# Performance work log

Measured on AMD Instinct MI355X. Metric: run time of the kernel, lower is better.

## Reference

```python
import jax, jax.numpy as jnp
import numpy as np

B, H, S, D = 4, 16, 2048, 64
SCALE = 8.0  # sqrt(D)
NEG = -1000000000.0


def setup_inputs() -> dict:
    key = jax.random.key(0)
    kq, kk, kv = jax.random.split(key, 3)
    q = jax.random.normal(kq, (B, H, S, D), dtype=jnp.float32)
    k = jax.random.normal(kk, (B, H, S, D), dtype=jnp.float32)
    v = jax.random.normal(kv, (B, H, S, D), dtype=jnp.float32)
    # causal mask: True means masked out (matches torch masked_fill)
    mask = jnp.triu(jnp.ones((S, S), dtype=bool), k=1)[None, None, :, :]
    mask = jnp.broadcast_to(mask, (B, 1, S, S))
    return {"q": q, "k": k, "v": v, "mask": mask}


def reference(q, k, v, mask):
    # score = q @ k^T / scale  -> [B,H,S,S]
    score = jnp.einsum("bhqd,bhkd->bhqk", q, k) / SCALE
    score = jnp.where(mask, NEG, score)
    probs = jax.nn.softmax(score, axis=-1)
    context = jnp.einsum("bhqk,bhkd->bhqd", probs, v)
    return context
```

## Files before the change

kernel.cpp:

```cpp
#include <hip/hip_runtime.h>

#define SQ 2048
#define DH 64
#define BK 64
#define NQT 32
#define NBH 64
#define M0 8.0f

#define WS_BYTES ((size_t)2 * NBH * SQ * DH * 2)

typedef float f32x4 __attribute__((ext_vector_type(4)));
typedef __bf16 bf16x8 __attribute__((ext_vector_type(8)));
typedef _Float16 f16x4 __attribute__((ext_vector_type(4)));
typedef _Float16 f16x8 __attribute__((ext_vector_type(8)));
typedef __fp16 fp16x2 __attribute__((ext_vector_type(2)));
typedef unsigned short u16x8 __attribute__((ext_vector_type(8)));
typedef unsigned int u32x4 __attribute__((ext_vector_type(4)));

#define WAIT_VM(N) asm volatile("s_waitcnt vmcnt(" #N ")" ::: "memory")

static __device__ __forceinline__ unsigned int pkbf(float a, float b) {
#if __has_builtin(__builtin_amdgcn_cvt_pk_bf16_f32)
  typedef __bf16 bf16x2 __attribute__((ext_vector_type(2)));
  bf16x2 r = __builtin_amdgcn_cvt_pk_bf16_f32(a, b);
  return __builtin_bit_cast(unsigned int, r);
#else
  unsigned int ua = __builtin_bit_cast(unsigned int, a);
  unsigned int ub = __builtin_bit_cast(unsigned int, b);
  ua += 0x7fffu + ((ua >> 16) & 1u);
  ub += 0x7fffu + ((ub >> 16) & 1u);
  return (ua >> 16) | (ub & 0xffff0000u);
#endif
}

static __device__ __forceinline__ unsigned int pkf16(float a, float b) {
  fp16x2 r = __builtin_amdgcn_cvt_pkrtz(a, b);
  return __builtin_bit_cast(unsigned int, r);
}

static __device__ __forceinline__ f32x4 mfma_qk(u16x8 a, u16x8 b, f32x4 c) {
  return __builtin_amdgcn_mfma_f32_16x16x32_bf16(
      __builtin_bit_cast(bf16x8, a), __builtin_bit_cast(bf16x8, b), c, 0, 0, 0);
}

static __device__ __forceinline__ f32x4 mfma_pv(f16x4 a, f16x4 b, f32x4 c) {
  return __builtin_amdgcn_mfma_f32_16x16x16f16(a, b, c, 0, 0, 0);
}

static __device__ __forceinline__ f32x4 mfma_pv32(f16x8 a, f16x8 b, f32x4 c) {
  return __builtin_amdgcn_mfma_f32_16x16x32_f16(a, b, c, 0, 0, 0);
}

static __device__ __forceinline__ void ld16(unsigned short* l, const unsigned short* g) {
  __builtin_amdgcn_global_load_lds(
      (const __attribute__((address_space(1))) unsigned int*)(const void*)g,
      (__attribute__((address_space(3))) unsigned int*)(void*)l, 16, 0, 0);
}

static __device__ __forceinline__ void store_tile(float* wb, float* dst,
                                                  const f32x4* o, int lane,
                                                  int l15, int quad) {
#pragma unroll
  for (int dt = 0; dt < 4; ++dt) {
    const int colw = dt * 16 + quad * 4;
    *(f32x4*)&wb[l15 * 64 + (colw ^ ((l15 & 3) * 16))] = o[dt];
  }
  __builtin_amdgcn_wave_barrier();
#pragma unroll
  for (int j = 0; j < 4; ++j) {
    const int row = j * 4 + (lane >> 4);
    const int colw = (lane & 15) * 4;
    f32x4 v = *(const f32x4*)&wb[row * 64 + (colw ^ ((row & 3) * 16))];
    *(f32x4*)&dst[row * 64 + colw] = v;
  }
}

__global__ __launch_bounds__(256) void prep(const float* __restrict__ K,
                                            const float* __restrict__ V,
                                            unsigned short* __restrict__ Kf,
                                            unsigned short* __restrict__ Vf) {
  const int bh = (int)blockIdx.x >> 5;
  const int st = (int)blockIdx.x & 31;
  const int tid = threadIdx.x;
  __shared__ __align__(16) unsigned short T[DH * 64];
  {
    const int kvb = (tid >> 4) * 4, vdb = (tid & 15) * 4;
    const float* vp = V + ((size_t)bh * SQ + st * 64 + kvb) * DH + vdb;
    f32x4 r0 = *(const f32x4*)vp, r1 = *(const f32x4*)(vp + DH),
          r2 = *(const f32x4*)(vp + 2 * DH), r3 = *(const f32x4*)(vp + 3 * DH);
    const int uu = kvb >> 3, h = (kvb >> 2) & 1;
#pragma unroll
    for (int i = 0; i < 4; ++i) {
      const int d = vdb + i;
      uint2 w = {pkf16(r0[i], r1[i]), pkf16(r2[i], r3[i])};
      *(uint2*)&T[d * 64 + ((uu ^ (d & 7)) * 8) + h * 4] = w;
    }
  }
  {
    const size_t kin = ((size_t)bh * SQ + st * 64) * DH;
    unsigned short* kfo = Kf + (size_t)bh * SQ * DH + (size_t)st * 64 * DH;
#pragma unroll
    for (int e = 0; e < 2; ++e) {
      const int L = tid * 2 + e;
      const int l15 = L & 15, quad = (L >> 4) & 3, c = (L >> 6) & 1, nt = (L >> 7) & 3;
      const int krow = (nt >> 1) * 32 + ((l15 >> 2) & 3) * 8 + (nt & 1) * 4 + (l15 & 3);
      const float* kp = K + kin + (size_t)krow * DH + (c * 4 + quad) * 8;
      f32x4 x = *(const f32x4*)kp, y = *(const f32x4*)(kp + 4);
      u32x4 w = {pkbf(x[0], x[1]), pkbf(x[2], x[3]), pkbf(y[0], y[1]), pkbf(y[2], y[3])};
      *(u32x4*)&kfo[L * 8] = w;
    }
  }
  __syncthreads();
  {
    unsigned short* vfo = Vf + (size_t)bh * SQ * DH + (size_t)st * 64 * DH;
#pragma unroll
    for (int e = 0; e < 2; ++e) {
      const int L = tid * 2 + e;
      const int l15 = L & 15, quad = (L >> 4) & 3, dt = (L >> 6) & 3, n2 = (L >> 8) & 1;
      const int d = dt * 16 + l15, uu = n2 * 4 + quad;
      u16x8 val = *(const u16x8*)&T[d * 64 + ((uu ^ (d & 7)) * 8)];
      *(u16x8*)&vfo[L * 8] = val;
    }
  }
}

__global__ __launch_bounds__(256, 2) void fa_main(
    const float* __restrict__ Q, const unsigned short* __restrict__ Kf,
    const unsigned short* __restrict__ Vf, float* __restrict__ O) {
  const int lin = (int)blockIdx.x;
  const int xcd = lin & 7, u = lin >> 3;
  const int hh = u & 7, j = u >> 3;
  const int bh = hh * 8 + xcd;

  const int tid = threadIdx.x;
  const int wv = tid >> 6;
  const int lane = tid & 63;
  const int l15 = lane & 15;
  const int quad = lane >> 4;

  const int p0 = j * 4 + wv;

  __shared__ __align__(16) unsigned short KS[4][2][4096];

  const size_t hq = (size_t)bh * (SQ * DH);
  const unsigned short* KfH = Kf + (size_t)bh * SQ * DH;
  const unsigned short* VfH = Vf + (size_t)bh * SQ * DH;

  const f16x8 ones8 = {(_Float16)1.f, (_Float16)1.f, (_Float16)1.f, (_Float16)1.f,
                       (_Float16)1.f, (_Float16)1.f, (_Float16)1.f, (_Float16)1.f};

  auto stageK = [&](int slot, int t) {
#pragma unroll
    for (int i = 0; i < 8; ++i)
      ld16(&KS[wv][slot][i * 512 + lane * 8],
           &KfH[(size_t)t * 4096 + i * 512 + lane * 8]);
  };

  auto run = [&](int s) {
    const int sg = s >> 1;
    const int qb = s * 32;
    const int qo = (s & 1) * 32;

    u16x8 qf[2][2];
    {
      const float scq = 0.125f * 1.4426950408889634f;
#pragma unroll
      for (int f = 0; f < 2; ++f) {
        const float* qp = Q + hq + (size_t)(qb + 16 * f + l15) * DH + quad * 8;
#pragma unroll
        for (int c = 0; c < 2; ++c) {
          f32x4 x = *(const f32x4*)(qp + c * 32);
          f32x4 y = *(const f32x4*)(qp + c * 32 + 4);
          u32x4 w = {pkbf(x[0] * scq, x[1] * scq), pkbf(x[2] * scq, x[3] * scq),
                     pkbf(y[0] * scq, y[1] * scq), pkbf(y[2] * scq, y[3] * scq)};
          qf[f][c] = __builtin_bit_cast(u16x8, w);
        }
      }
    }

    f32x4 o0[4], o1[4], la0, la1;
#pragma unroll
    for (int dt = 0; dt < 4; ++dt) {
      o0[dt] = (f32x4){0.f, 0.f, 0.f, 0.f};
      o1[dt] = (f32x4){0.f, 0.f, 0.f, 0.f};
    }
    la0 = (f32x4){0.f, 0.f, 0.f, 0.f};
    la1 = (f32x4){0.f, 0.f, 0.f, 0.f};

    f16x8 vb[8];
    auto loadV = [&](int t) {
#pragma unroll
      for (int i = 0; i < 8; ++i)
        vb[i] = *(const f16x8*)&VfH[(size_t)t * 4096 + i * 512 + lane * 8];
    };

    auto attend = [&](const unsigned short* Ks, bool diag) {
      f32x4 s0[4], s1[4];
#pragma unroll
      for (int nt = 0; nt < 4; ++nt) {
        f32x4 a0 = {-M0, -M0, -M0, -M0}, a1 = {-M0, -M0, -M0, -M0};
#pragma unroll
        for (int c = 0; c < 2; ++c) {
          u16x8 kf = *(const u16x8*)&Ks[(nt * 2 + c) * 512 + lane * 8];
          a0 = mfma_qk(kf, qf[0][c], a0);
          a1 = mfma_qk(kf, qf[1][c], a1);
        }
        s0[nt] = a0;
        s1[nt] = a1;
      }
      if (diag) {
#pragma unroll
        for (int nt = 0; nt < 4; ++nt)
#pragma unroll
          for (int r = 0; r < 4; ++r) {
            const int kvl = (nt >> 1) * 32 + quad * 8 + (nt & 1) * 4 + r;
            if (kvl > qo + l15) s0[nt][r] = -1e30f;
            if (kvl > qo + 16 + l15) s1[nt][r] = -1e30f;
          }
      }
      f16x8 pf0[2], pf1[2];
#pragma unroll
      for (int n2 = 0; n2 < 2; ++n2) {
        f32x4 pe0, po0, pe1, po1;
#pragma unroll
        for (int r = 0; r < 4; ++r) {
          pe0[r] = __builtin_amdgcn_exp2f(s0[2 * n2][r]);
          po0[r] = __builtin_amdgcn_exp2f(s0[2 * n2 + 1][r]);
          pe1[r] = __builtin_amdgcn_exp2f(s1[2 * n2][r]);
          po1[r] = __builtin_amdgcn_exp2f(s1[2 * n2 + 1][r]);
        }
        u32x4 w0 = {pkf16(pe0[0], pe0[1]), pkf16(pe0[2], pe0[3]),
                    pkf16(po0[0], po0[1]), pkf16(po0[2], po0[3])};
        u32x4 w1 = {pkf16(pe1[0], pe1[1]), pkf16(pe1[2], pe1[3]),
                    pkf16(po1[0], po1[1]), pkf16(po1[2], po1[3])};
        pf0[n2] = __builtin_bit_cast(f16x8, w0);
        pf1[n2] = __builtin_bit_cast(f16x8, w1);
      }
#pragma unroll
      for (int n2 = 0; n2 < 2; ++n2) {
        la0 = mfma_pv32(ones8, pf0[n2], la0);
        la1 = mfma_pv32(ones8, pf1[n2], la1);
      }
#pragma unroll
      for (int dt = 0; dt < 4; ++dt) {
#pragma unroll
        for (int n2 = 0; n2 < 2; ++n2) {
          const f16x8 vf = vb[n2 * 4 + dt];
          o0[dt] = mfma_pv32(vf, pf0[n2], o0[dt]);
          o1[dt] = mfma_pv32(vf, pf1[n2], o1[dt]);
        }
      }
    };

    stageK(0, 0);
    loadV(0);
    if (sg >= 1) stageK(1, 1);

    for (int t = 0; t <= sg; ++t) {
      if (t < sg) {
        WAIT_VM(8);
      } else {
        WAIT_VM(0);
      }
      __builtin_amdgcn_sched_barrier(0);
      attend(&KS[wv][t & 1][0], t == sg);
      __builtin_amdgcn_sched_barrier(0);
      if (t + 1 <= sg) loadV(t + 1);
      if (t + 2 <= sg) stageK(t & 1, t + 2);
    }

    {
      const float inv0 = 1.0f / la0[0];
      const float inv1 = 1.0f / la1[0];
#pragma unroll
      for (int f = 0; f < 2; ++f) {
        const f32x4* oo = f ? o1 : o0;
        const float inv = f ? inv1 : inv0;
        float* dst = O + hq + (size_t)(qb + f * 16 + l15) * DH + quad * 4;
#pragma unroll
        for (int dt = 0; dt < 4; ++dt) {
          f32x4 v = oo[dt] * inv;
          *(f32x4*)(dst + dt * 16) = v;
        }
      }
    }
  };

  run(p0);
  run(63 - p0);
}

__global__ __launch_bounds__(256, 4) void fa_full(
    const float* __restrict__ Q, const float* __restrict__ K,
    const float* __restrict__ V, float* __restrict__ O) {
  const int lin = (int)blockIdx.x;
  const int xcd = lin & 7;
  const int u = lin >> 3;
  const int hh = u & 7;
  const int p = u >> 3;
  const int bh = hh * 8 + xcd;
  const int tid = threadIdx.x;
  const int wv = tid >> 6;
  const int lane = tid & 63;
  const int l15 = lane & 15;
  const int quad = lane >> 4;
  __shared__ __align__(16) unsigned short SMEM[2][2 * BK * DH];
  const size_t hbase = (size_t)bh * (SQ * DH);
  const int krr = tid >> 3, kcc = (tid & 7) * 8;
  const int kvb = (tid >> 4) * 4, vdb = (tid & 15) * 4;
#pragma unroll
  for (int ph = 0; ph < 2; ++ph) {
    const int qt = ph ? (NQT - 1 - p) : p;
    const int wq0 = qt * 64 + wv * 16;
    u16x8 qf[2];
    {
      const float scq = 0.125f * 1.4426950408889634f;
      const float* qp = Q + hbase + (size_t)(wq0 + l15) * DH + quad * 8;
#pragma unroll
      for (int c = 0; c < 2; ++c) {
        f32x4 x = *(const f32x4*)(qp + c * 32);
        f32x4 y = *(const f32x4*)(qp + c * 32 + 4);
        u32x4 w = {pkbf(x[0] * scq, x[1] * scq), pkbf(x[2] * scq, x[3] * scq),
                   pkbf(y[0] * scq, y[1] * scq), pkbf(y[2] * scq, y[3] * scq)};
        qf[c] = __builtin_bit_cast(u16x8, w);
      }
    }
    f32x4 o[4];
#pragma unroll
    for (int dt = 0; dt < 4; ++dt) o[dt] = (f32x4){0.f, 0.f, 0.f, 0.f};
    float l = 0.f;
    f32x4 ka[2][2], va[4];
    {
      const float* kp = K + hbase + (size_t)krr * DH + kcc;
      ka[0][0] = *(const f32x4*)kp;             ka[0][1] = *(const f32x4*)(kp + 4);
      ka[1][0] = *(const f32x4*)(kp + 32 * DH); ka[1][1] = *(const f32x4*)(kp + 32 * DH + 4);
      const float* vp = V + hbase + (size_t)kvb * DH + vdb;
      va[0] = *(const f32x4*)vp;            va[1] = *(const f32x4*)(vp + DH);
      va[2] = *(const f32x4*)(vp + 2 * DH); va[3] = *(const f32x4*)(vp + 3 * DH);
    }
    __syncthreads();
    {
      unsigned short* Ksn = SMEM[0];
      unsigned short* Vsn = SMEM[0] + BK * DH;
#pragma unroll
      for (int h = 0; h < 2; ++h) {
        const int rr = h * 32 + krr;
        u32x4 w = {pkbf(ka[h][0][0], ka[h][0][1]), pkbf(ka[h][0][2], ka[h][0][3]),
                   pkbf(ka[h][1][0], ka[h][1][1]), pkbf(ka[h][1][2], ka[h][1][3])};
        *(u32x4*)&Ksn[rr * DH + (kcc ^ ((rr & 7) * 8))] = w;
      }
#pragma unroll
      for (int i = 0; i < 4; ++i) {
        const int d = vdb + i;
        uint2 w = {pkf16(va[0][i], va[1][i]), pkf16(va[2][i], va[3][i])};
        *(uint2*)&Vsn[d * BK + (kvb ^ ((d & 15) * 4))] = w;
      }
    }
    __syncthreads();
    for (int t = 0; t <= qt; ++t) {
      const unsigned short* Ks = SMEM[t & 1];
      const unsigned short* Vs = SMEM[t & 1] + BK * DH;
      if (t < qt) {
        const int kb2 = (t + 1) * BK;
        const float* kp = K + hbase + (size_t)(kb2 + krr) * DH + kcc;
        ka[0][0] = *(const f32x4*)kp;             ka[0][1] = *(const f32x4*)(kp + 4);
        ka[1][0] = *(const f32x4*)(kp + 32 * DH); ka[1][1] = *(const f32x4*)(kp + 32 * DH + 4);
        const float* vp = V + hbase + (size_t)(kb2 + kvb) * DH + vdb;
        va[0] = *(const f32x4*)vp;            va[1] = *(const f32x4*)(vp + DH);
        va[2] = *(const f32x4*)(vp + 2 * DH); va[3] = *(const f32x4*)(vp + 3 * DH);
      }
      f32x4 s[4];
#pragma unroll
      for (int nt = 0; nt < 4; ++nt) {
        f32x4 acc = {-M0, -M0, -M0, -M0};
#pragma unroll
        for (int c = 0; c < 2; ++c) {
          const int row = nt * 16 + l15;
          u16x8 kf = *(const u16x8*)&Ks[row * DH + ((c * 32 + quad * 8) ^ ((l15 & 7) * 8))];
          acc = mfma_qk(kf, qf[c], acc);
        }
        s[nt] = acc;
      }
      if (t == qt) {
#pragma unroll
        for (int nt = 0; nt < 4; ++nt)
#pragma unroll
          for (int r = 0; r < 4; ++r)
            if (nt * 16 + quad * 4 + r > wv * 16 + l15) s[nt][r] = -1e30f;
      }
      f16x4 pf[4];
#pragma unroll
      for (int nt = 0; nt < 4; ++nt) {
        f32x4 pr;
#pragma unroll
        for (int r = 0; r < 4; ++r) { pr[r] = __builtin_amdgcn_exp2f(s[nt][r]); l += pr[r]; }
        uint2 w2 = {pkf16(pr[0], pr[1]), pkf16(pr[2], pr[3])};
        pf[nt] = __builtin_bit_cast(f16x4, w2);
      }
#pragma unroll
      for (int dt = 0; dt < 4; ++dt) {
        const int d = dt * 16 + l15;
#pragma unroll
        for (int nt = 0; nt < 4; ++nt) {
          f16x4 vf = *(const f16x4*)&Vs[d * BK + ((nt * 16 + quad * 4) ^ (l15 * 4))];
          o[dt] = mfma_pv(vf, pf[nt], o[dt]);
        }
      }
      if (t < qt) {
        unsigned short* Ksn = SMEM[(t + 1) & 1];
        unsigned short* Vsn = SMEM[(t + 1) & 1] + BK * DH;
#pragma unroll
        for (int h = 0; h < 2; ++h) {
          const int rr = h * 32 + krr;
          u32x4 w = {pkbf(ka[h][0][0], ka[h][0][1]), pkbf(ka[h][0][2], ka[h][0][3]),
                     pkbf(ka[h][1][0], ka[h][1][1]), pkbf(ka[h][1][2], ka[h][1][3])};
          *(u32x4*)&Ksn[rr * DH + (kcc ^ ((rr & 7) * 8))] = w;
        }
#pragma unroll
        for (int i = 0; i < 4; ++i) {
          const int d = vdb + i;
          uint2 w = {pkf16(va[0][i], va[1][i]), pkf16(va[2][i], va[3][i])};
          *(uint2*)&Vsn[d * BK + (kvb ^ ((d & 15) * 4))] = w;
        }
        __syncthreads();
      }
    }
    l += __shfl_xor(l, 16, 64);
    l += __shfl_xor(l, 32, 64);
    const float inv = 1.0f / l;
    f32x4 on[4];
#pragma unroll
    for (int dt = 0; dt < 4; ++dt) on[dt] = o[dt] * inv;
    float* wb = (float*)SMEM[(qt + 1) & 1] + wv * 1024;
    store_tile(wb, O + hbase + (size_t)wq0 * DH, on, lane, l15, quad);
  }
}

extern "C" void kernel_launch(void* const* d_in, const int* in_sizes, int n_in,
                              void* d_out, int out_size, void* d_ws, size_t ws_size,
                              hipStream_t stream) {
  const float* q = (const float*)d_in[0];
  const float* k = (const float*)d_in[1];
  const float* v = (const float*)d_in[2];
  float* o = (float*)d_out;
  if (ws_size >= WS_BYTES) {
    unsigned short* Kf = (unsigned short*)d_ws;
    unsigned short* Vf = Kf + (size_t)NBH * SQ * DH;
    prep<<<dim3(NBH * 32), 256, 0, stream>>>(k, v, Kf, Vf);
    fa_main<<<dim3(512), 256, 0, stream>>>(q, Kf, Vf, o);
  } else {
    fa_full<<<dim3(1024), 256, 0, stream>>>(q, k, v, o);
  }
}
```

Before: 210.5 us.

## Share K tiles across waves with cooperative 4-slot LDS ring and 1024 blocks

Restructures fa_main so each block handles one 128-row query tile, with its four waves covering consecutive 32-row strips, instead of each wave independently running two paired strips. K tiles are now loaded cooperatively by all waves into a shared 4-slot LDS ring guarded by block barriers, and V is double-buffered in registers. The grid doubles to 1024 blocks with occupancy hint 4, and a lookup constant orders tiles longest-first for load balance. This cuts redundant K loads and per-wave LDS use. In exchange it adds block-wide barriers and creates imbalance between waves inside a block, since waves with shorter causal ranges sit idle.

```diff
diff --git a/kernel.cpp b/kernel.cpp
--- a/kernel.cpp
+++ b/kernel.cpp
@@ -124,13 +124,15 @@
   }
 }
 
-__global__ __launch_bounds__(256, 2) void fa_main(
+__global__ __launch_bounds__(256, 4) void fa_main(
     const float* __restrict__ Q, const unsigned short* __restrict__ Kf,
     const unsigned short* __restrict__ Vf, float* __restrict__ O) {
   const int lin = (int)blockIdx.x;
   const int xcd = lin & 7, u = lin >> 3;
-  const int hh = u & 7, j = u >> 3;
+  const int hh = u & 7;
+  const int pi = (int)((0x32104567BA98CDEFull >> ((u >> 3) * 4)) & 15u);
   const int bh = hh * 8 + xcd;
+  const int tend = 2 * pi + 1;
 
   const int tid = threadIdx.x;
   const int wv = tid >> 6;
@@ -138,156 +140,158 @@
   const int l15 = lane & 15;
   const int quad = lane >> 4;
 
-  const int p0 = j * 4 + wv;
-
-  __shared__ __align__(16) unsigned short KS[4][2][4096];
+  __shared__ __align__(16) unsigned short KB[4][4096];
 
   const size_t hq = (size_t)bh * (SQ * DH);
   const unsigned short* KfH = Kf + (size_t)bh * SQ * DH;
   const unsigned short* VfH = Vf + (size_t)bh * SQ * DH;
 
+  const int qbase = pi * 128 + wv * 32;
+  const int dtw = 2 * pi + (wv >> 1);
+  const int qo = (wv & 1) * 32;
+
+  u16x8 qf[2][2];
+  {
+    const float scq = 0.125f * 1.4426950408889634f;
+#pragma unroll
+    for (int f = 0; f < 2; ++f) {
+      const float* qp = Q + hq + (size_t)(qbase + 16 * f + l15) * DH + quad * 8;
+#pragma unroll
+      for (int c = 0; c < 2; ++c) {
+        f32x4 x = *(const f32x4*)(qp + c * 32);
+        f32x4 y = *(const f32x4*)(qp + c * 32 + 4);
+        u32x4 w = {pkbf(x[0] * scq, x[1] * scq), pkbf(x[2] * scq, x[3] * scq),
+                   pkbf(y[0] * scq, y[1] * scq), pkbf(y[2] * scq, y[3] * scq)};
+        qf[f][c] = __builtin_bit_cast(u16x8, w);
+      }
+    }
+  }
+
+  f32x4 o0[4], o1[4], la0, la1;
+#pragma unroll
+  for (int dt = 0; dt < 4; ++dt) {
+    o0[dt] = (f32x4){0.f, 0.f, 0.f, 0.f};
+    o1[dt] = (f32x4){0.f, 0.f, 0.f, 0.f};
+  }
+  la0 = (f32x4){0.f, 0.f, 0.f, 0.f};
+  la1 = (f32x4){0.f, 0.f, 0.f, 0.f};
   const f16x8 ones8 = {(_Float16)1.f, (_Float16)1.f, (_Float16)1.f, (_Float16)1.f,
                        (_Float16)1.f, (_Float16)1.f, (_Float16)1.f, (_Float16)1.f};
 
-  auto stageK = [&](int slot, int t) {
+  f16x8 vbA[8], vbB[8];
+  auto loadV = [&](f16x8* vb, int t) {
 #pragma unroll
     for (int i = 0; i < 8; ++i)
-      ld16(&KS[wv][slot][i * 512 + lane * 8],
-           &KfH[(size_t)t * 4096 + i * 512 + lane * 8]);
+      vb[i] = *(const f16x8*)&VfH[(size_t)t * 4096 + i * 512 + lane * 8];
   };
-
-  auto run = [&](int s) {
-    const int sg = s >> 1;
-    const int qb = s * 32;
-    const int qo = (s & 1) * 32;
-
-    u16x8 qf[2][2];
-    {
-      const float scq = 0.125f * 1.4426950408889634f;
-#pragma unroll
-      for (int f = 0; f < 2; ++f) {
-        const float* qp = Q + hq + (size_t)(qb + 16 * f + l15) * DH + quad * 8;
-#pragma unroll
-        for (int c = 0; c < 2; ++c) {
-          f32x4 x = *(const f32x4*)(qp + c * 32);
-          f32x4 y = *(const f32x4*)(qp + c * 32 + 4);
-          u32x4 w = {pkbf(x[0] * scq, x[1] * scq), pkbf(x[2] * scq, x[3] * scq),
-                     pkbf(y[0] * scq, y[1] * scq), pkbf(y[2] * scq, y[3] * scq)};
-          qf[f][c] = __builtin_bit_cast(u16x8, w);
+  auto stageK = [&](int t) {
+    unsigned short* W = KB[t & 3];
+#pragma unroll
+    for (int j = 0; j < 2; ++j) {
+      const int off = wv * 1024 + j * 512 + lane * 8;
+      ld16(&W[off], &KfH[(size_t)t * 4096 + off]);
+    }
+  };
+
+  auto attend = [&](int t, const f16x8* vb, bool diag) {
+    const unsigned short* Ks = KB[t & 3];
+    f32x4 s0[4], s1[4];
+#pragma unroll
+    for (int nt = 0; nt < 4; ++nt) {
+      f32x4 a0 = {-M0, -M0, -M0, -M0}, a1 = {-M0, -M0, -M0, -M0};
+#pragma unroll
+      for (int c = 0; c < 2; ++c) {
+        u16x8 kf = *(const u16x8*)&Ks[(nt * 2 + c) * 512 + lane * 8];
+        a0 = mfma_qk(kf, qf[0][c], a0);
+        a1 = mfma_qk(kf, qf[1][c], a1);
+      }
+      s0[nt] = a0;
+      s1[nt] = a1;
+    }
+    if (diag) {
+#pragma unroll
+      for (int nt = 0; nt < 4; ++nt)
+#pragma unroll
+        for (int r = 0; r < 4; ++r) {
+          const int kvl = (nt >> 1) * 32 + quad * 8 + (nt & 1) * 4 + r;
+          if (kvl > qo + l15) s0[nt][r] = -1e30f;
+          if (kvl > qo + 16 + l15) s1[nt][r] = -1e30f;
         }
-      }
-    }
-
-    f32x4 o0[4], o1[4], la0, la1;
+    }
+    f16x8 pf0[2], pf1[2];
+#pragma unroll
+    for (int n2 = 0; n2 < 2; ++n2) {
+      f32x4 pe0, po0, pe1, po1;
+#pragma unroll
+      for (int r = 0; r < 4; ++r) {
+        pe0[r] = __builtin_amdgcn_exp2f(s0[2 * n2][r]);
+        po0[r] = __builtin_amdgcn_exp2f(s0[2 * n2 + 1][r]);
+        pe1[r] = __builtin_amdgcn_exp2f(s1[2 * n2][r]);
+        po1[r] = __builtin_amdgcn_exp2f(s1[2 * n2 + 1][r]);
+      }
+      u32x4 w0 = {pkf16(pe0[0], pe0[1]), pkf16(pe0[2], pe0[3]),
+                  pkf16(po0[0], po0[1]), pkf16(po0[2], po0[3])};
+      u32x4 w1 = {pkf16(pe1[0], pe1[1]), pkf16(pe1[2], pe1[3]),
+                  pkf16(po1[0], po1[1]), pkf16(po1[2], po1[3])};
+      pf0[n2] = __builtin_bit_cast(f16x8, w0);
+      pf1[n2] = __builtin_bit_cast(f16x8, w1);
+    }
+#pragma unroll
+    for (int n2 = 0; n2 < 2; ++n2) {
+      la0 = mfma_pv32(ones8, pf0[n2], la0);
+      la1 = mfma_pv32(ones8, pf1[n2], la1);
+    }
 #pragma unroll
     for (int dt = 0; dt < 4; ++dt) {
-      o0[dt] = (f32x4){0.f, 0.f, 0.f, 0.f};
-      o1[dt] = (f32x4){0.f, 0.f, 0.f, 0.f};
-    }
-    la0 = (f32x4){0.f, 0.f, 0.f, 0.f};
-    la1 = (f32x4){0.f, 0.f, 0.f, 0.f};
-
-    f16x8 vb[8];
-    auto loadV = [&](int t) {
-#pragma unroll
-      for (int i = 0; i < 8; ++i)
-        vb[i] = *(const f16x8*)&VfH[(size_t)t * 4096 + i * 512 + lane * 8];
-    };
-
-    auto attend = [&](const unsigned short* Ks, bool diag) {
-      f32x4 s0[4], s1[4];
-#pragma unroll
-      for (int nt = 0; nt < 4; ++nt) {
-        f32x4 a0 = {-M0, -M0, -M0, -M0}, a1 = {-M0, -M0, -M0, -M0};
-#pragma unroll
-        for (int c = 0; c < 2; ++c) {
-          u16x8 kf = *(const u16x8*)&Ks[(nt * 2 + c) * 512 + lane * 8];
-          a0 = mfma_qk(kf, qf[0][c], a0);
-          a1 = mfma_qk(kf, qf[1][c], a1);
-        }
-        s0[nt] = a0;
-        s1[nt] = a1;
-      }
-      if (diag) {
-#pragma unroll
-        for (int nt = 0; nt < 4; ++nt)
-#pragma unroll
-          for (int r = 0; r < 4; ++r) {
-            const int kvl = (nt >> 1) * 32 + quad * 8 + (nt & 1) * 4 + r;
-            if (kvl > qo + l15) s0[nt][r] = -1e30f;
-            if (kvl > qo + 16 + l15) s1[nt][r] = -1e30f;
-          }
-      }
-      f16x8 pf0[2], pf1[2];
 #pragma unroll
       for (int n2 = 0; n2 < 2; ++n2) {
-        f32x4 pe0, po0, pe1, po1;
-#pragma unroll
-        for (int r = 0; r < 4; ++r) {
-          pe0[r] = __builtin_amdgcn_exp2f(s0[2 * n2][r]);
-          po0[r] = __builtin_amdgcn_exp2f(s0[2 * n2 + 1][r]);
-          pe1[r] = __builtin_amdgcn_exp2f(s1[2 * n2][r]);
-          po1[r] = __builtin_amdgcn_exp2f(s1[2 * n2 + 1][r]);
-        }
-        u32x4 w0 = {pkf16(pe0[0], pe0[1]), pkf16(pe0[2], pe0[3]),
-                    pkf16(po0[0], po0[1]), pkf16(po0[2], po0[3])};
-        u32x4 w1 = {pkf16(pe1[0], pe1[1]), pkf16(pe1[2], pe1[3]),
-                    pkf16(po1[0], po1[1]), pkf16(po1[2], po1[3])};
-        pf0[n2] = __builtin_bit_cast(f16x8, w0);
-        pf1[n2] = __builtin_bit_cast(f16x8, w1);
-      }
-#pragma unroll
-      for (int n2 = 0; n2 < 2; ++n2) {
-        la0 = mfma_pv32(ones8, pf0[n2], la0);
-        la1 = mfma_pv32(ones8, pf1[n2], la1);
-      }
+        const f16x8 vf = vb[n2 * 4 + dt];
+        o0[dt] = mfma_pv32(vf, pf0[n2], o0[dt]);
+        o1[dt] = mfma_pv32(vf, pf1[n2], o1[dt]);
+      }
+    }
+  };
+
+  stageK(0);
+  stageK(1);
+  loadV(vbA, 0);
+  loadV(vbB, 1);
+  WAIT_VM(0);
+  __builtin_amdgcn_s_barrier();
+  __builtin_amdgcn_sched_barrier(0);
+
+  for (int t = 0; t <= tend; t += 2) {
+    if (t + 2 <= tend) stageK(t + 2);
+    if (t + 3 <= tend) stageK(t + 3);
+    if (t <= dtw) attend(t, vbA, t == dtw);
+    if (t + 2 <= tend) loadV(vbA, t + 2);
+    if (t + 1 <= dtw) attend(t + 1, vbB, t + 1 == dtw);
+    if (t + 3 <= tend) loadV(vbB, t + 3);
+    if (t + 2 > tend) break;
+    if (t + 3 <= tend) {
+      WAIT_VM(16);
+    } else {
+      WAIT_VM(8);
+    }
+    __builtin_amdgcn_s_barrier();
+    __builtin_amdgcn_sched_barrier(0);
+  }
+
+  {
+    const float inv0 = 1.0f / la0[0];
+    const float inv1 = 1.0f / la1[0];
+#pragma unroll
+    for (int f = 0; f < 2; ++f) {
+      const f32x4* oo = f ? o1 : o0;
+      const float inv = f ? inv1 : inv0;
+      float* dst = O + hq + (size_t)(qbase + f * 16 + l15) * DH + quad * 4;
 #pragma unroll
       for (int dt = 0; dt < 4; ++dt) {
-#pragma unroll
-        for (int n2 = 0; n2 < 2; ++n2) {
-          const f16x8 vf = vb[n2 * 4 + dt];
-          o0[dt] = mfma_pv32(vf, pf0[n2], o0[dt]);
-          o1[dt] = mfma_pv32(vf, pf1[n2], o1[dt]);
-        }
-      }
-    };
-
-    stageK(0, 0);
-    loadV(0);
-    if (sg >= 1) stageK(1, 1);
-
-    for (int t = 0; t <= sg; ++t) {
-      if (t < sg) {
-        WAIT_VM(8);
-      } else {
-        WAIT_VM(0);
-      }
-      __builtin_amdgcn_sched_barrier(0);
-      attend(&KS[wv][t & 1][0], t == sg);
-      __builtin_amdgcn_sched_barrier(0);
-      if (t + 1 <= sg) loadV(t + 1);
-      if (t + 2 <= sg) stageK(t & 1, t + 2);
-    }
-
-    {
-      const float inv0 = 1.0f / la0[0];
-      const float inv1 = 1.0f / la1[0];
-#pragma unroll
-      for (int f = 0; f < 2; ++f) {
-        const f32x4* oo = f ? o1 : o0;
-        const float inv = f ? inv1 : inv0;
-        float* dst = O + hq + (size_t)(qb + f * 16 + l15) * DH + quad * 4;
-#pragma unroll
-        for (int dt = 0; dt < 4; ++dt) {
-          f32x4 v = oo[dt] * inv;
-          *(f32x4*)(dst + dt * 16) = v;
-        }
-      }
-    }
-  };
-
-  run(p0);
-  run(63 - p0);
+        f32x4 v = oo[dt] * inv;
+        *(f32x4*)(dst + dt * 16) = v;
+      }
+    }
+  }
 }
 
 __global__ __launch_bounds__(256, 4) void fa_full(
@@ -447,7 +451,7 @@
     unsigned short* Kf = (unsigned short*)d_ws;
     unsigned short* Vf = Kf + (size_t)NBH * SQ * DH;
     prep<<<dim3(NBH * 32), 256, 0, stream>>>(k, v, Kf, Vf);
-    fa_main<<<dim3(512), 256, 0, stream>>>(q, Kf, Vf, o);
+    fa_main<<<dim3(1024), 256, 0, stream>>>(q, Kf, Vf, o);
   } else {
     fa_full<<<dim3(1024), 256, 0, stream>>>(q, k, v, o);
   }
```

After: 322.1 us. 53.0% more time.
